# Kernel optimization log

Measured on AMD Instinct MI355X. Metric: run time of the kernel, lower is better.

Reference implementation:

```python
import jax, jax.numpy as jnp
import numpy as np

N_NODES = 50000


def setup_inputs() -> dict:
    key = jax.random.key(0)
    k1, k2, k3, k4 = jax.random.split(key, 4)
    in_dim, out_dim, n_edges = 128, 64, 800000
    x = jax.random.normal(k1, (N_NODES, in_dim), dtype=jnp.float32)
    edge_index = jax.random.randint(k2, (2, n_edges), 0, N_NODES, dtype=jnp.int64)
    W = jax.random.normal(k3, (in_dim, out_dim), dtype=jnp.float32) * (1.0 / np.sqrt(in_dim))
    att = jax.random.normal(k4, (2 * out_dim,), dtype=jnp.float32) * (1.0 / np.sqrt(2 * out_dim))
    return {"x": x, "edge_index": edge_index, "W": W, "att": att}


def reference(x, edge_index, W, att):
    N = x.shape[0]
    F_out = W.shape[1]
    h = x @ W                                   # [N, F]
    src, dst = edge_index[0], edge_index[1]
    hs = h[src]                                 # [E, F] gather
    hd = h[dst]                                 # [E, F] gather
    # att(cat([h_src, h_dst])) == h_src @ a1 + h_dst @ a2
    a1, a2 = att[:F_out], att[F_out:]
    logit = jax.nn.leaky_relu(hs @ a1 + hd @ a2, 0.2)   # [E]
    E = logit.shape[0]
    # The original builds a dense [N, E] matrix (row d holds logit_e at col e
    # for dst[e]==d, zeros elsewhere) and softmaxes over the E axis. The
    # equivalent sparse form: denom_d = sum_{e:dst=d} exp(logit_e) + (E - deg_d)*exp(0),
    # stabilized with m_d = max(max logit over segment, 0).
    seg_max = jax.ops.segment_max(logit, dst, num_segments=N)      # -inf on empty
    m = jnp.maximum(seg_max, 0.0)                                  # include the zero cells
    exp_l = jnp.exp(logit - m[dst])                                # [E]
    seg_sum = jax.ops.segment_sum(exp_l, dst, num_segments=N)      # [N]
    deg = jax.ops.segment_sum(jnp.ones_like(logit), dst, num_segments=N)
    denom = seg_sum + (jnp.float32(E) - deg) * jnp.exp(-m)         # zeros' contribution
    w = exp_l / denom[dst]                                          # [E]
    agg = jax.ops.segment_sum(w[:, None] * hs, dst, num_segments=N)  # [N, F]
    return jax.nn.elu(agg)
```

## Files before the change

### kernel.cpp

```cpp
#include <hip/hip_runtime.h>
#include <hip/hip_bf16.h>

#define FIN 128
#define FOUT 64
#define BINW 128
#define NBINPAD 512
#define QS 2560
#define TILE 4096
#define DPQ 32
#define RCAP 768

typedef __attribute__((ext_vector_type(8))) short short8;
typedef __attribute__((ext_vector_type(4))) float f32x4;
typedef __attribute__((ext_vector_type(8))) _Float16 h8;

__device__ __forceinline__ unsigned short f2bf(float f) {
    unsigned u = __float_as_uint(f);
    unsigned r = u + 0x7FFFu + ((u >> 16) & 1u);
    return (unsigned short)(r >> 16);
}

__global__ __launch_bounds__(256) void k_prep(
    const float* __restrict__ W, const float* __restrict__ att,
    unsigned short* __restrict__ Whig, unsigned short* __restrict__ Wlog,
    float* __restrict__ wag, int* __restrict__ qcur, int nzero)
{
    const int t = threadIdx.x;
    if (blockIdx.x >= 65) {
        const int i = (blockIdx.x - 65) * 256 + t;
        if (i < nzero) qcur[i] = 0;
        return;
    }
    if (blockIdx.x == 64) {
        const int k = t & 127, which = t >> 7;
        const float* av = att + which * 64;
        const float* wr = W + k * 64;
        float acc = 0.f;
        #pragma unroll 16
        for (int n = 0; n < 64; ++n) acc += wr[n] * av[n];
        wag[which * 128 + k] = acc;
        return;
    }
    const int f = blockIdx.x * 256 + t;
    const int combo = f >> 9;
    const int s = combo >> 2, c = combo & 3;
    const int r = f & 511;
    const int l = r >> 3, j = r & 7;
    const int k = s * 32 + (l >> 4) * 8 + j;
    const int n = c * 16 + (l & 15);
    const float w = W[k * 64 + n];
    const unsigned short hi = f2bf(w);
    const float hif = __uint_as_float((unsigned)hi << 16);
    Whig[f] = hi;
    Wlog[f] = f2bf(w - hif);
}

__global__ __launch_bounds__(256) void k_fused(
    const float* __restrict__ x, const unsigned short* __restrict__ Whig,
    const unsigned short* __restrict__ Wlog, const float* __restrict__ wag,
    _Float16* __restrict__ h, float* __restrict__ as_, float* __restrict__ ad_,
    const int* __restrict__ src, const int* __restrict__ dst,
    unsigned* __restrict__ queue, int* __restrict__ qcur,
    int N, int E, int nbins, int paBlocks)
{
    union SMem {
        struct { unsigned rec[TILE]; int hist[NBINPAD]; int scanb[NBINPAD];
                 int excl[NBINPAD]; int gb[NBINPAD]; } pa;
    };
    __shared__ SMem sm;
    const int t = threadIdx.x;

    if ((int)blockIdx.x < paBlocks) {
        const int e0 = blockIdx.x * TILE;
        const int tot = (E - e0 < TILE) ? (E - e0) : TILE;
        sm.pa.hist[t] = 0; sm.pa.hist[t + 256] = 0;
        __syncthreads();
        #pragma unroll
        for (int i = 0; i < TILE / 256; ++i) {
            const int e = e0 + i * 256 + t;
            if (e < E) atomicAdd(&sm.pa.hist[__builtin_nontemporal_load(dst + e) >> 7], 1);
        }
        __syncthreads();
        const int v0 = sm.pa.hist[t], v1 = sm.pa.hist[t + 256];
        sm.pa.scanb[t] = v0; sm.pa.scanb[t + 256] = v1;
        __syncthreads();
        #pragma unroll
        for (int off = 1; off < NBINPAD; off <<= 1) {
            const int a0 = (t >= off) ? sm.pa.scanb[t - off] : 0;
            const int a1 = (t + 256 >= off) ? sm.pa.scanb[t + 256 - off] : 0;
            __syncthreads();
            sm.pa.scanb[t] += a0; sm.pa.scanb[t + 256] += a1;
            __syncthreads();
        }
        const int ex0 = sm.pa.scanb[t] - v0;
        const int ex1 = sm.pa.scanb[t + 256] - v1;
        int g0 = 0, g1 = 0;
        if (t < nbins && v0 > 0)       g0 = t * QS + atomicAdd(qcur + t, v0);
        if (t + 256 < nbins && v1 > 0) g1 = (t + 256) * QS + atomicAdd(qcur + t + 256, v1);
        sm.pa.hist[t] = ex0; sm.pa.hist[t + 256] = ex1;
        sm.pa.excl[t] = ex0; sm.pa.excl[t + 256] = ex1;
        sm.pa.gb[t] = g0;   sm.pa.gb[t + 256] = g1;
        __syncthreads();
        #pragma unroll
        for (int i = 0; i < TILE / 256; ++i) {
            const int e = e0 + i * 256 + t;
            if (e < E) {
                const int d = __builtin_nontemporal_load(dst + e);
                const int s = __builtin_nontemporal_load(src + e);
                const int pos = atomicAdd(&sm.pa.hist[d >> 7], 1);
                sm.pa.rec[pos] = (unsigned)s | ((unsigned)d << 16);
            }
        }
        __syncthreads();
        for (int i = t; i < tot; i += 256) {
            const unsigned r = sm.pa.rec[i];
            const int b = (int)(r >> 23);
            const int gpos = sm.pa.gb[b] + (i - sm.pa.excl[b]);
            if (gpos < (b + 1) * QS) queue[gpos] = r;
        }
        return;
    }

    const int bb = blockIdx.x - paBlocks;
    const int wv = t >> 6, lane = t & 63;
    const int quad = lane >> 4, mrow = lane & 15;
    const int r0 = (bb * 4 + wv) * 16;
    const int arow = r0 + mrow;
    const bool rok = arow < N;

    f32x4 acc[4] = {};
    float s1 = 0.f, s2 = 0.f;

    #pragma unroll
    for (int s = 0; s < 4; ++s) {
        float xv[8];
        if (rok) {
            const float4* p = (const float4*)(x + (size_t)arow * FIN + s * 32 + quad * 8);
            const float4 u0 = p[0], u1 = p[1];
            xv[0] = u0.x; xv[1] = u0.y; xv[2] = u0.z; xv[3] = u0.w;
            xv[4] = u1.x; xv[5] = u1.y; xv[6] = u1.z; xv[7] = u1.w;
        } else {
            #pragma unroll
            for (int j = 0; j < 8; ++j) xv[j] = 0.f;
        }
        const float4 wa0 = *(const float4*)&wag[s * 32 + quad * 8];
        const float4 wa1 = *(const float4*)&wag[s * 32 + quad * 8 + 4];
        const float4 wb0 = *(const float4*)&wag[128 + s * 32 + quad * 8];
        const float4 wb1 = *(const float4*)&wag[128 + s * 32 + quad * 8 + 4];
        const float wva[8] = {wa0.x, wa0.y, wa0.z, wa0.w, wa1.x, wa1.y, wa1.z, wa1.w};
        const float wvb[8] = {wb0.x, wb0.y, wb0.z, wb0.w, wb1.x, wb1.y, wb1.z, wb1.w};

        short8 ah, al;
        #pragma unroll
        for (int j = 0; j < 8; ++j) {
            s1 += xv[j] * wva[j];
            s2 += xv[j] * wvb[j];
            const unsigned short hi = f2bf(xv[j]);
            const float hif = __uint_as_float((unsigned)hi << 16);
            ah[j] = (short)hi;
            al[j] = (short)f2bf(xv[j] - hif);
        }
        #pragma unroll
        for (int c = 0; c < 4; ++c) {
            const short8 bh = *(const short8*)&Whig[((s * 4 + c) * 64 + lane) * 8];
            const short8 bl = *(const short8*)&Wlog[((s * 4 + c) * 64 + lane) * 8];
            acc[c] = __builtin_amdgcn_mfma_f32_16x16x32_bf16(ah, bh, acc[c], 0, 0, 0);
            acc[c] = __builtin_amdgcn_mfma_f32_16x16x32_bf16(al, bh, acc[c], 0, 0, 0);
            acc[c] = __builtin_amdgcn_mfma_f32_16x16x32_bf16(ah, bl, acc[c], 0, 0, 0);
        }
    }

    s1 += __shfl_xor(s1, 16); s1 += __shfl_xor(s1, 32);
    s2 += __shfl_xor(s2, 16); s2 += __shfl_xor(s2, 32);
    if (lane < 16 && r0 + lane < N) {
        as_[r0 + lane] = s1;
        ad_[r0 + lane] = s2;
    }

    #pragma unroll
    for (int reg = 0; reg < 4; ++reg) {
        const int orow = r0 + quad * 4 + reg;
        if (orow < N) {
            #pragma unroll
            for (int c = 0; c < 4; ++c)
                h[(size_t)orow * FOUT + c * 16 + mrow] = (_Float16)acc[c][reg];
        }
    }
}

__global__ __launch_bounds__(256) void k_aggq(
    const int* __restrict__ qcur, const unsigned* __restrict__ queue,
    const float* __restrict__ as_, const float* __restrict__ ad_,
    const _Float16* __restrict__ h, float* __restrict__ out,
    int N, float Ef)
{
    __shared__ unsigned rec[RCAP];
    __shared__ unsigned pay[RCAP];
    __shared__ int hist[DPQ], base[DPQ], cur[DPQ];
    __shared__ float adl[DPQ];
    __shared__ int nloc;

    const int bin = blockIdx.x >> 2, q = blockIdx.x & 3;
    const int d0 = bin * BINW + q * DPQ;
    const int t = threadIdx.x;
    const int wv = t >> 6, lane = t & 63;

    if (t < DPQ) {
        hist[t] = 0;
        const int d = d0 + t;
        adl[t] = (d < N) ? ad_[d] : 0.f;
    }
    if (t == 0) nloc = 0;
    __syncthreads();

    int cnt = qcur[bin];
    if (cnt > QS) cnt = QS;

    for (int i = t; i < cnt; i += 256) {
        const unsigned r = __builtin_nontemporal_load(queue + (size_t)bin * QS + i);
        if ((int)((r >> 21) & 3) == q) {
            const int p = atomicAdd(&nloc, 1);
            if (p < RCAP) rec[p] = r;
        }
    }
    __syncthreads();
    int n = nloc; if (n > RCAP) n = RCAP;

    for (int i = t; i < n; i += 256) atomicAdd(&hist[(rec[i] >> 16) & (DPQ - 1)], 1);
    __syncthreads();

    if (t < DPQ) base[t] = hist[t];
    __syncthreads();
    #pragma unroll
    for (int off = 1; off < DPQ; off <<= 1) {
        const int a = (t < DPQ && t >= off) ? base[t - off] : 0;
        __syncthreads();
        if (t < DPQ) base[t] += a;
        __syncthreads();
    }
    if (t < DPQ) { base[t] -= hist[t]; cur[t] = base[t]; }
    __syncthreads();

    for (int i = t; i < n; i += 256) {
        const unsigned r = rec[i];
        const int s  = (int)(r & 0xFFFFu);
        const int dl = (int)(r >> 16) & (DPQ - 1);
        const float z = as_[s] + adl[dl];
        const float lg = (z >= 0.f) ? z : 0.2f * z;
        const int pos = atomicAdd(&cur[dl], 1);
        pay[pos] = (unsigned)s |
            ((unsigned)__builtin_bit_cast(unsigned short, (_Float16)lg) << 16);
    }
    __syncthreads();

    const int e8 = lane >> 3, ch = lane & 7;
    for (int dl = wv; dl < DPQ; dl += 4) {
        const int d = d0 + dl;
        if (d >= N) continue;
        const int dg = hist[dl];
        const int bs = base[dl];

        float mx = -INFINITY;
        for (int j = lane; j < dg; j += 64)
            mx = fmaxf(mx, (float)__builtin_bit_cast(_Float16,
                          (unsigned short)(pay[bs + j] >> 16)));
        #pragma unroll
        for (int off = 32; off > 0; off >>= 1) mx = fmaxf(mx, __shfl_xor(mx, off));
        const float m = fmaxf(mx, 0.f);

        float ss = 0.f;
        for (int j = lane; j < dg; j += 64)
            ss += expf((float)__builtin_bit_cast(_Float16,
                       (unsigned short)(pay[bs + j] >> 16)) - m);
        #pragma unroll
        for (int off = 32; off > 0; off >>= 1) ss += __shfl_xor(ss, off);
        const float inv = 1.f / (ss + (Ef - (float)dg) * expf(-m));

        float acc[8];
        #pragma unroll
        for (int k = 0; k < 8; ++k) acc[k] = 0.f;

        for (int jb = 0; jb < dg; jb += 16) {
            const int j0 = jb + e8, j1 = jb + 8 + e8;
            float w0 = 0.f, w1 = 0.f; int s0 = 0, s1 = 0;
            if (j0 < dg) {
                const unsigned p = pay[bs + j0];
                s0 = (int)(p & 0xFFFFu);
                w0 = expf((float)__builtin_bit_cast(_Float16,
                          (unsigned short)(p >> 16)) - m) * inv;
            }
            if (j1 < dg) {
                const unsigned p = pay[bs + j1];
                s1 = (int)(p & 0xFFFFu);
                w1 = expf((float)__builtin_bit_cast(_Float16,
                          (unsigned short)(p >> 16)) - m) * inv;
            }
            const h8 hv0 = *(const h8*)(h + (size_t)s0 * FOUT + ch * 8);
            const h8 hv1 = *(const h8*)(h + (size_t)s1 * FOUT + ch * 8);
            #pragma unroll
            for (int k = 0; k < 8; ++k)
                acc[k] += w0 * (float)hv0[k] + w1 * (float)hv1[k];
        }

        #pragma unroll
        for (int k = 0; k < 8; ++k) {
            acc[k] += __shfl_xor(acc[k], 8);
            acc[k] += __shfl_xor(acc[k], 16);
            acc[k] += __shfl_xor(acc[k], 32);
        }
        if (lane < 8) {
            float r[8];
            #pragma unroll
            for (int k = 0; k < 8; ++k) r[k] = (acc[k] > 0.f) ? acc[k] : expm1f(acc[k]);
            float4* op = (float4*)(out + (size_t)d * FOUT + lane * 8);
            op[0] = make_float4(r[0], r[1], r[2], r[3]);
            op[1] = make_float4(r[4], r[5], r[6], r[7]);
        }
    }
}

extern "C" void kernel_launch(void* const* d_in, const int* in_sizes, int n_in,
                              void* d_out, int out_size, void* d_ws, size_t ws_size,
                              hipStream_t stream) {
    const float* x   = (const float*)d_in[0];
    const int*   ei  = (const int*)d_in[1];
    const float* W   = (const float*)d_in[2];
    const float* att = (const float*)d_in[3];

    const int N = in_sizes[0] / FIN;
    const int E = in_sizes[1] / 2;
    const int* src = ei;
    const int* dst = ei + E;

    const int NBINS = (N + BINW - 1) / BINW;

    char* ws = (char*)d_ws;
    size_t o = 0;
    auto carve = [&](size_t bytes) {
        void* p = ws + o; o += (bytes + 1023) & ~(size_t)1023; return p;
    };
    unsigned short* Whig = (unsigned short*)carve(16384 * 2);
    unsigned short* Wlog = (unsigned short*)carve(16384 * 2);
    float*          wag  = (float*)carve(256 * 4);
    float*          as_  = (float*)carve((size_t)N * 4);
    float*          ad_  = (float*)carve((size_t)N * 4);
    int*            qcur = (int*)carve((size_t)NBINS * 4);
    _Float16*       h    = (_Float16*)carve((size_t)N * FOUT * 2);
    unsigned*       queue = (unsigned*)carve((size_t)NBINS * QS * 4);

    float* out = (float*)d_out;

    const int paBlocks = (E + TILE - 1) / TILE;
    const int mmBlocks = (N + 63) / 64;
    const int zBlks    = (NBINS + 255) / 256;

    k_prep<<<65 + zBlks, 256, 0, stream>>>(W, att, Whig, Wlog, wag, qcur, NBINS);
    k_fused<<<paBlocks + mmBlocks, 256, 0, stream>>>(
        x, Whig, Wlog, wag, h, as_, ad_, src, dst, queue, qcur, N, E, NBINS, paBlocks);
    k_aggq<<<NBINS * 4, 256, 0, stream>>>(qcur, queue, as_, ad_, h, out, N, (float)E);
}
```

Before: 152.0 us.

## Enlarge partition tile, merge offset tables, ballot-aggregate atomics, cache exp weights

Doubles the edge tile per partition block so fewer blocks hit the global bin counters. The two per-bin shared tables collapse into one combined offset, and queue writes become nontemporal stores. In the aggregation kernel, per-lane shared atomics on the record counter are replaced by one wave-level ballot/popcount atomic, and exp weights are cached in shared memory so they are not recomputed. Costs are more shared memory (larger LDS footprint, possibly lower occupancy), fewer partition blocks, and dropped unroll pragmas.

```diff
diff --git a/kernel.cpp b/kernel.cpp
--- a/kernel.cpp
+++ b/kernel.cpp
@@ -6,7 +6,7 @@
 #define BINW 128
 #define NBINPAD 512
 #define QS 2560
-#define TILE 4096
+#define TILE 8192
 #define DPQ 32
 #define RCAP 768
 
@@ -65,7 +65,7 @@
 {
     union SMem {
         struct { unsigned rec[TILE]; int hist[NBINPAD]; int scanb[NBINPAD];
-                 int excl[NBINPAD]; int gb[NBINPAD]; } pa;
+                 int comb[NBINPAD]; } pa;
     };
     __shared__ SMem sm;
     const int t = threadIdx.x;
@@ -75,7 +75,6 @@
         const int tot = (E - e0 < TILE) ? (E - e0) : TILE;
         sm.pa.hist[t] = 0; sm.pa.hist[t + 256] = 0;
         __syncthreads();
-        #pragma unroll
         for (int i = 0; i < TILE / 256; ++i) {
             const int e = e0 + i * 256 + t;
             if (e < E) atomicAdd(&sm.pa.hist[__builtin_nontemporal_load(dst + e) >> 7], 1);
@@ -94,14 +93,14 @@
         }
         const int ex0 = sm.pa.scanb[t] - v0;
         const int ex1 = sm.pa.scanb[t + 256] - v1;
-        int g0 = 0, g1 = 0;
-        if (t < nbins && v0 > 0)       g0 = t * QS + atomicAdd(qcur + t, v0);
-        if (t + 256 < nbins && v1 > 0) g1 = (t + 256) * QS + atomicAdd(qcur + t + 256, v1);
+        int c0 = 0, c1 = 0;
+        if (t < nbins && v0 > 0)
+            c0 = t * QS + atomicAdd(qcur + t, v0) - ex0;
+        if (t + 256 < nbins && v1 > 0)
+            c1 = (t + 256) * QS + atomicAdd(qcur + t + 256, v1) - ex1;
         sm.pa.hist[t] = ex0; sm.pa.hist[t + 256] = ex1;
-        sm.pa.excl[t] = ex0; sm.pa.excl[t + 256] = ex1;
-        sm.pa.gb[t] = g0;   sm.pa.gb[t + 256] = g1;
-        __syncthreads();
-        #pragma unroll
+        sm.pa.comb[t] = c0;  sm.pa.comb[t + 256] = c1;
+        __syncthreads();
         for (int i = 0; i < TILE / 256; ++i) {
             const int e = e0 + i * 256 + t;
             if (e < E) {
@@ -115,8 +114,9 @@
         for (int i = t; i < tot; i += 256) {
             const unsigned r = sm.pa.rec[i];
             const int b = (int)(r >> 23);
-            const int gpos = sm.pa.gb[b] + (i - sm.pa.excl[b]);
-            if (gpos < (b + 1) * QS) queue[gpos] = r;
+            const int gpos = sm.pa.comb[b] + i;
+            if (gpos < (b + 1) * QS)
+                __builtin_nontemporal_store(r, queue + gpos);
         }
         return;
     }
@@ -196,6 +196,7 @@
 {
     __shared__ unsigned rec[RCAP];
     __shared__ unsigned pay[RCAP];
+    __shared__ float wexp[RCAP];
     __shared__ int hist[DPQ], base[DPQ], cur[DPQ];
     __shared__ float adl[DPQ];
     __shared__ int nloc;
@@ -218,8 +219,13 @@
 
     for (int i = t; i < cnt; i += 256) {
         const unsigned r = __builtin_nontemporal_load(queue + (size_t)bin * QS + i);
-        if ((int)((r >> 21) & 3) == q) {
-            const int p = atomicAdd(&nloc, 1);
+        const bool m = ((int)((r >> 21) & 3) == q);
+        const unsigned long long mk = __ballot(m);
+        int b0 = 0;
+        if (lane == 0 && mk) b0 = atomicAdd(&nloc, __popcll(mk));
+        b0 = __shfl(b0, 0);
+        if (m) {
+            const int p = b0 + __popcll(mk & ((1ull << lane) - 1ull));
             if (p < RCAP) rec[p] = r;
         }
     }
@@ -269,9 +275,12 @@
         const float m = fmaxf(mx, 0.f);
 
         float ss = 0.f;
-        for (int j = lane; j < dg; j += 64)
-            ss += expf((float)__builtin_bit_cast(_Float16,
+        for (int j = lane; j < dg; j += 64) {
+            const float e = expf((float)__builtin_bit_cast(_Float16,
                        (unsigned short)(pay[bs + j] >> 16)) - m);
+            wexp[bs + j] = e;
+            ss += e;
+        }
         #pragma unroll
         for (int off = 32; off > 0; off >>= 1) ss += __shfl_xor(ss, off);
         const float inv = 1.f / (ss + (Ef - (float)dg) * expf(-m));
@@ -284,16 +293,12 @@
             const int j0 = jb + e8, j1 = jb + 8 + e8;
             float w0 = 0.f, w1 = 0.f; int s0 = 0, s1 = 0;
             if (j0 < dg) {
-                const unsigned p = pay[bs + j0];
-                s0 = (int)(p & 0xFFFFu);
-                w0 = expf((float)__builtin_bit_cast(_Float16,
-                          (unsigned short)(p >> 16)) - m) * inv;
+                s0 = (int)(pay[bs + j0] & 0xFFFFu);
+                w0 = wexp[bs + j0] * inv;
             }
             if (j1 < dg) {
-                const unsigned p = pay[bs + j1];
-                s1 = (int)(p & 0xFFFFu);
-                w1 = expf((float)__builtin_bit_cast(_Float16,
-                          (unsigned short)(p >> 16)) - m) * inv;
+                s1 = (int)(pay[bs + j1] & 0xFFFFu);
+                w1 = wexp[bs + j1] * inv;
             }
             const h8 hv0 = *(const h8*)(h + (size_t)s0 * FOUT + ch * 8);
             const h8 hv1 = *(const h8*)(h + (size_t)s1 * FOUT + ch * 8);
```

Measured after the change: 163.8 us. +7.7%, slower.
